# Kernel tuning notes

Measured on AMD Instinct MI355X. Metric: run time of the kernel, lower is better.

Reference implementation:

```python
import jax, jax.numpy as jnp
from jax import lax
import numpy as np

PATCH_H = 8
PATCH_W = 8


def setup_inputs() -> dict:
    key = jax.random.key(0)
    k1, k2 = jax.random.split(key)
    x = jax.random.normal(k1, (2, 1024, 256, 256), dtype=jnp.float32)
    # Conv1d weight [C_out, C_in, k], bias=False
    conv_w = jax.random.normal(k2, (1024, 1024, 3), dtype=jnp.float32) * 0.02
    return {"x": x, "conv_w": conv_w}


def reference(x, conv_w):
    B, C, H, W = x.shape
    hf, wf = H // PATCH_H, W // PATCH_W
    P = hf * wf
    # Patch average pool: mean over each (PATCH_H, PATCH_W) tile -> [B, C, hf, wf]
    xp = x.reshape(B, C, hf, PATCH_H, wf, PATCH_W)
    y = xp.mean(axis=(3, 5)).reshape(B, C, P)
    # Conv1d over the patch axis (SAME padding, no bias), then sigmoid gate
    g = lax.conv_general_dilated(
        y, conv_w, window_strides=(1,), padding="SAME",
        dimension_numbers=("NCH", "OIH", "NCH"))
    g = jax.nn.sigmoid(g).reshape(B, C, hf, wf)
    # Broadcast gate back over each patch and multiply
    out = xp * g[:, :, :, None, :, None]
    return out.reshape(B, C, H, W)
```

## Files before the change

### kernel.cpp

```cpp
#include <hip/hip_runtime.h>
#include <hip/hip_bf16.h>

#define HH 256
#define WW 256
#define CCH 1024
#define PP 1024

using f32x4 = __attribute__((ext_vector_type(4))) float;
using short8 = __attribute__((ext_vector_type(8))) short;

__global__ __launch_bounds__(256) void pool_kernel(const float* __restrict__ x,
                                                   float* __restrict__ y) {
    int bc   = blockIdx.x;
    int wid  = threadIdx.x >> 6;
    int lane = threadIdx.x & 63;
    const float* xp = x + (size_t)bc * (HH * WW) + lane * 4;
    float* yp = y + (size_t)bc * PP;
#pragma unroll
    for (int s = 0; s < 8; ++s) {
        int ph = wid + s * 4;
        const float* slab = xp + (size_t)ph * 8 * WW;
        float acc = 0.f;
#pragma unroll
        for (int r = 0; r < 8; ++r) {
            f32x4 v = __builtin_nontemporal_load((const f32x4*)(slab + (size_t)r * WW));
            acc += v.x + v.y + v.z + v.w;
        }
        acc += __shfl_xor(acc, 1);
        if ((lane & 1) == 0)
            yp[ph * 32 + (lane >> 1)] = acc * (1.f / 64.f);
    }
}

__global__ __launch_bounds__(256) void wconv_pad_kernel(const float* __restrict__ w,
                                                        __hip_bfloat16* __restrict__ wT,
                                                        __hip_bfloat16* __restrict__ yT) {
    int tid = blockIdx.x * 256 + threadIdx.x;
    const float* p = w + (size_t)tid * 3;
    float a = p[0], b = p[1], c = p[2];
    wT[tid]               = __float2bfloat16(a);
    wT[(1u << 20) + tid]  = __float2bfloat16(b);
    wT[(2u << 20) + tid]  = __float2bfloat16(c);
    if (tid < 2 * CCH) {
        int bb = tid >> 10, cc = tid & 1023;
        __hip_bfloat16 z = __float2bfloat16(0.f);
        __hip_bfloat16* base = yT + (size_t)bb * (PP + 2) * CCH;
        base[cc] = z;
        base[(size_t)(PP + 1) * CCH + cc] = z;
    }
}

__global__ __launch_bounds__(256) void transpose_kernel(const float* __restrict__ y,
                                                        __hip_bfloat16* __restrict__ yT) {
    int b  = blockIdx.z;
    int c0 = blockIdx.x * 32;
    int p0 = blockIdx.y * 32;
    __shared__ float tile[32][33];
    int tx = threadIdx.x, ty = threadIdx.y;
    const float* yb = y + (size_t)b * CCH * PP;
#pragma unroll
    for (int rr = 0; rr < 4; ++rr)
        tile[ty + rr * 8][tx] = yb[(size_t)(c0 + ty + rr * 8) * PP + p0 + tx];
    __syncthreads();
    __hip_bfloat16* yTb = yT + (size_t)b * (PP + 2) * CCH;
#pragma unroll
    for (int rr = 0; rr < 4; ++rr)
        yTb[(size_t)(1 + p0 + ty + rr * 8) * CCH + c0 + tx] =
            __float2bfloat16(tile[tx][ty + rr * 8]);
}

__global__ __launch_bounds__(512) void conv_gemm_kernel(
        const __hip_bfloat16* __restrict__ wT,
        const __hip_bfloat16* __restrict__ yT,
        float* __restrict__ gate) {
    int lane = threadIdx.x & 63;
    int wid  = threadIdx.x >> 6;
    int wp  = wid & 1, wco = wid >> 1;
    int l15 = lane & 15, lhi = lane >> 4;
    int co_base = blockIdx.x * 64 + wco * 16;
    int p_base  = blockIdx.y * 64 + wp * 32;
    int b = blockIdx.z;
    const __hip_bfloat16* yTb = yT + (size_t)b * (PP + 2) * CCH;

    f32x4 acc[2] = {};
#pragma unroll
    for (int tap = 0; tap < 3; ++tap) {
        const __hip_bfloat16* Ap = wT + (size_t)tap * (1u << 20)
                                 + (size_t)(co_base + l15) * CCH + lhi * 8;
        const __hip_bfloat16* Bp = yTb + (size_t)(p_base + l15 + tap) * CCH + lhi * 8;
        for (int ci0 = 0; ci0 < CCH; ci0 += 32) {
            short8 a0 = *(const short8*)(Ap + ci0);
            short8 b0 = *(const short8*)(Bp + ci0);
            short8 b1 = *(const short8*)(Bp + ci0 + 16 * CCH);
            acc[0] = __builtin_amdgcn_mfma_f32_16x16x32_bf16(a0, b0, acc[0], 0, 0, 0);
            acc[1] = __builtin_amdgcn_mfma_f32_16x16x32_bf16(a0, b1, acc[1], 0, 0, 0);
        }
    }
    float* gb = gate + (size_t)b * CCH * PP;
#pragma unroll
    for (int j16 = 0; j16 < 2; ++j16) {
        int col  = p_base + j16 * 16 + l15;
        int row0 = co_base + lhi * 4;
#pragma unroll
        for (int r = 0; r < 4; ++r) {
            float v = acc[j16][r];
            gb[(size_t)(row0 + r) * PP + col] = 1.f / (1.f + __expf(-v));
        }
    }
}

__global__ __launch_bounds__(256) void apply_kernel(const float* __restrict__ x,
                                                    const float* __restrict__ gate,
                                                    float* __restrict__ out) {
    int bc = blockIdx.x;
    const float* xp = x   + (size_t)bc * (HH * WW);
    float*       op = out + (size_t)bc * (HH * WW);
    __shared__ float g[PP];
    int t = threadIdx.x;
    ((f32x4*)g)[t] = ((const f32x4*)(gate + (size_t)bc * PP))[t];
    __syncthreads();
    int col4 = t & 63;
    int r    = t >> 6;
    int pc   = col4 >> 1;
#pragma unroll 4
    for (int it = 0; it < 64; ++it) {
        int row = it * 4 + r;
        float gg = g[(row >> 3) * 32 + pc];
        size_t off = (size_t)row * 64 + col4;
        f32x4 v = __builtin_nontemporal_load((const f32x4*)xp + off);
        v *= gg;
        __builtin_nontemporal_store(v, (f32x4*)op + off);
    }
}

extern "C" void kernel_launch(void* const* d_in, const int* in_sizes, int n_in,
                              void* d_out, int out_size, void* d_ws, size_t ws_size,
                              hipStream_t stream) {
    const float* x = (const float*)d_in[0];
    const float* w = (const float*)d_in[1];
    float* out = (float*)d_out;

    char* ws = (char*)d_ws;
    float*          y    = (float*)(ws);
    __hip_bfloat16* yT   = (__hip_bfloat16*)(ws + 8388608);
    __hip_bfloat16* wT   = (__hip_bfloat16*)(ws + 12591104);
    float*          gate = (float*)(ws + 18882560);

    hipLaunchKernelGGL(pool_kernel,      dim3(2048),      dim3(256),   0, stream, x, y);
    hipLaunchKernelGGL(wconv_pad_kernel, dim3(4096),      dim3(256),   0, stream, w, wT, yT);
    hipLaunchKernelGGL(transpose_kernel, dim3(32, 32, 2), dim3(32, 8), 0, stream, y, yT);
    hipLaunchKernelGGL(conv_gemm_kernel, dim3(16, 16, 2), dim3(512),   0, stream, wT, yT, gate);
    hipLaunchKernelGGL(apply_kernel,     dim3(2048),      dim3(256),   0, stream, x, gate, out);
}
```

Baseline: 427.2 us.

## Fuse all stages into one cooperative persistent kernel with grid syncs

Replaces the five separate kernel launches with a single cooperative kernel of 256 blocks that runs pooling, weight conversion, transpose, the MFMA conv GEMM and the gated apply in sequence, separated by grid.sync barriers. The aim is to remove per-launch overhead and inter-kernel gaps. In exchange the grid drops to 256 persistent blocks, which lowers parallelism in the memory-bound pool and apply phases, and each grid barrier adds its own cost. If the cooperative launch fails, the code falls back to the original launches.

```diff
diff --git a/kernel.cpp b/kernel.cpp
--- a/kernel.cpp
+++ b/kernel.cpp
@@ -1,5 +1,6 @@
 #include <hip/hip_runtime.h>
 #include <hip/hip_bf16.h>
+#include <hip/hip_cooperative_groups.h>
 
 #define HH 256
 #define WW 256
@@ -8,6 +9,147 @@
 
 using f32x4 = __attribute__((ext_vector_type(4))) float;
 using short8 = __attribute__((ext_vector_type(8))) short;
+
+namespace cg = cooperative_groups;
+
+__global__ __launch_bounds__(512, 2) void fused_kernel(
+        const float* __restrict__ x, const float* __restrict__ w,
+        float* __restrict__ out,
+        float* __restrict__ y, __hip_bfloat16* __restrict__ yT,
+        __hip_bfloat16* __restrict__ wT, float* __restrict__ gate) {
+    cg::grid_group grid = cg::this_grid();
+    __shared__ __align__(16) float lds[32 * 33];
+
+    const int bid  = blockIdx.x;
+    const int t    = threadIdx.x;
+    const int wid  = t >> 6;
+    const int lane = t & 63;
+
+    {
+        int plane = bid * 8 + wid;
+        const float* xp = x + (size_t)plane * (HH * WW) + lane * 4;
+        float* yp = y + (size_t)plane * PP;
+#pragma unroll 2
+        for (int ph = 0; ph < 32; ++ph) {
+            const float* slab = xp + (size_t)ph * 8 * WW;
+            float acc = 0.f;
+#pragma unroll
+            for (int r = 0; r < 8; ++r) {
+                f32x4 v = __builtin_nontemporal_load((const f32x4*)(slab + (size_t)r * WW));
+                acc += v.x + v.y + v.z + v.w;
+            }
+            acc += __shfl_xor(acc, 1);
+            if ((lane & 1) == 0)
+                yp[ph * 32 + (lane >> 1)] = acc * (1.f / 64.f);
+        }
+    }
+    {
+#pragma unroll
+        for (int it = 0; it < 8; ++it) {
+            int idx = it * (1 << 17) + bid * 512 + t;
+            const float* p = w + (size_t)idx * 3;
+            wT[idx]             = __float2bfloat16(p[0]);
+            wT[(1 << 20) + idx] = __float2bfloat16(p[1]);
+            wT[(2 << 20) + idx] = __float2bfloat16(p[2]);
+        }
+        int g0 = bid * 512 + t;
+        if (g0 < 2 * CCH) {
+            int bb = g0 >> 10, cc = g0 & 1023;
+            __hip_bfloat16 z = __float2bfloat16(0.f);
+            __hip_bfloat16* base = yT + (size_t)bb * (PP + 2) * CCH;
+            base[cc] = z;
+            base[(size_t)(PP + 1) * CCH + cc] = z;
+        }
+    }
+    __threadfence();
+    grid.sync();
+
+    {
+        int tx = t & 31, ty = t >> 5;
+#pragma unroll 1
+        for (int i = 0; i < 8; ++i) {
+            int tt = bid * 8 + i;
+            int b = tt >> 10, rem = tt & 1023;
+            int c0 = (rem >> 5) * 32, p0 = (rem & 31) * 32;
+            const float* yb = y + (size_t)b * CCH * PP;
+#pragma unroll
+            for (int rr = 0; rr < 2; ++rr)
+                lds[(ty + rr * 16) * 33 + tx] = yb[(size_t)(c0 + ty + rr * 16) * PP + p0 + tx];
+            __syncthreads();
+            __hip_bfloat16* yTb = yT + (size_t)b * (PP + 2) * CCH;
+#pragma unroll
+            for (int rr = 0; rr < 2; ++rr)
+                yTb[(size_t)(1 + p0 + ty + rr * 16) * CCH + c0 + tx] =
+                    __float2bfloat16(lds[tx * 33 + ty + rr * 16]);
+            __syncthreads();
+        }
+    }
+    __threadfence();
+    grid.sync();
+
+    {
+        int wp = wid & 1, wco = wid >> 1;
+        int l15 = lane & 15, lhi = lane >> 4;
+#pragma unroll 1
+        for (int j = 0; j < 2; ++j) {
+            int job = bid * 2 + j;
+            int bx = job & 15, by = (job >> 4) & 15, bz = job >> 8;
+            int co_base = bx * 64 + wco * 16;
+            int p_base  = by * 64 + wp * 32;
+            const __hip_bfloat16* yTb = yT + (size_t)bz * (PP + 2) * CCH;
+            f32x4 acc[2] = {};
+#pragma unroll
+            for (int tap = 0; tap < 3; ++tap) {
+                const __hip_bfloat16* Ap = wT + (size_t)tap * (1u << 20)
+                                         + (size_t)(co_base + l15) * CCH + lhi * 8;
+                const __hip_bfloat16* Bp = yTb + (size_t)(p_base + l15 + tap) * CCH + lhi * 8;
+                for (int ci0 = 0; ci0 < CCH; ci0 += 32) {
+                    short8 a0 = *(const short8*)(Ap + ci0);
+                    short8 b0 = *(const short8*)(Bp + ci0);
+                    short8 b1 = *(const short8*)(Bp + ci0 + 16 * CCH);
+                    acc[0] = __builtin_amdgcn_mfma_f32_16x16x32_bf16(a0, b0, acc[0], 0, 0, 0);
+                    acc[1] = __builtin_amdgcn_mfma_f32_16x16x32_bf16(a0, b1, acc[1], 0, 0, 0);
+                }
+            }
+            float* gb = gate + (size_t)bz * CCH * PP;
+#pragma unroll
+            for (int j16 = 0; j16 < 2; ++j16) {
+                int col  = p_base + j16 * 16 + l15;
+                int row0 = co_base + lhi * 4;
+#pragma unroll
+                for (int r = 0; r < 4; ++r)
+                    gb[(size_t)(row0 + r) * PP + col] = 1.f / (1.f + __expf(-acc[j16][r]));
+            }
+        }
+    }
+    __threadfence();
+    grid.sync();
+
+    {
+        int col4 = t & 63;
+        int r    = t >> 6;
+        int pc   = col4 >> 1;
+#pragma unroll 1
+        for (int i = 0; i < 8; ++i) {
+            int plane = bid * 8 + i;
+            const float* xp = x   + (size_t)plane * (HH * WW);
+            float*       op = out + (size_t)plane * (HH * WW);
+            if (t < 256)
+                ((f32x4*)lds)[t] = ((const f32x4*)(gate + (size_t)plane * PP))[t];
+            __syncthreads();
+#pragma unroll 4
+            for (int it = 0; it < 32; ++it) {
+                int row = it * 8 + r;
+                float gg = lds[(row >> 3) * 32 + pc];
+                size_t off = (size_t)row * 64 + col4;
+                f32x4 v = __builtin_nontemporal_load((const f32x4*)xp + off);
+                v *= gg;
+                __builtin_nontemporal_store(v, (f32x4*)op + off);
+            }
+            __syncthreads();
+        }
+    }
+}
 
 __global__ __launch_bounds__(256) void pool_kernel(const float* __restrict__ x,
                                                    float* __restrict__ y) {
@@ -37,10 +179,9 @@
                                                         __hip_bfloat16* __restrict__ yT) {
     int tid = blockIdx.x * 256 + threadIdx.x;
     const float* p = w + (size_t)tid * 3;
-    float a = p[0], b = p[1], c = p[2];
-    wT[tid]               = __float2bfloat16(a);
-    wT[(1u << 20) + tid]  = __float2bfloat16(b);
-    wT[(2u << 20) + tid]  = __float2bfloat16(c);
+    wT[tid]               = __float2bfloat16(p[0]);
+    wT[(1u << 20) + tid]  = __float2bfloat16(p[1]);
+    wT[(2u << 20) + tid]  = __float2bfloat16(p[2]);
     if (tid < 2 * CCH) {
         int bb = tid >> 10, cc = tid & 1023;
         __hip_bfloat16 z = __float2bfloat16(0.f);
@@ -81,7 +222,6 @@
     int p_base  = blockIdx.y * 64 + wp * 32;
     int b = blockIdx.z;
     const __hip_bfloat16* yTb = yT + (size_t)b * (PP + 2) * CCH;
-
     f32x4 acc[2] = {};
 #pragma unroll
     for (int tap = 0; tap < 3; ++tap) {
@@ -102,10 +242,8 @@
         int col  = p_base + j16 * 16 + l15;
         int row0 = co_base + lhi * 4;
 #pragma unroll
-        for (int r = 0; r < 4; ++r) {
-            float v = acc[j16][r];
-            gb[(size_t)(row0 + r) * PP + col] = 1.f / (1.f + __expf(-v));
-        }
+        for (int r = 0; r < 4; ++r)
+            gb[(size_t)(row0 + r) * PP + col] = 1.f / (1.f + __expf(-acc[j16][r]));
     }
 }
 
@@ -146,9 +284,16 @@
     __hip_bfloat16* wT   = (__hip_bfloat16*)(ws + 12591104);
     float*          gate = (float*)(ws + 18882560);
 
-    hipLaunchKernelGGL(pool_kernel,      dim3(2048),      dim3(256),   0, stream, x, y);
-    hipLaunchKernelGGL(wconv_pad_kernel, dim3(4096),      dim3(256),   0, stream, w, wT, yT);
-    hipLaunchKernelGGL(transpose_kernel, dim3(32, 32, 2), dim3(32, 8), 0, stream, y, yT);
-    hipLaunchKernelGGL(conv_gemm_kernel, dim3(16, 16, 2), dim3(512),   0, stream, wT, yT, gate);
-    hipLaunchKernelGGL(apply_kernel,     dim3(2048),      dim3(256),   0, stream, x, gate, out);
-}
+    void* args[] = {(void*)&x, (void*)&w, (void*)&out,
+                    (void*)&y, (void*)&yT, (void*)&wT, (void*)&gate};
+    hipError_t err = hipLaunchCooperativeKernel((const void*)fused_kernel,
+                                                dim3(256), dim3(512), args, 0, stream);
+    if (err != hipSuccess) {
+        (void)hipGetLastError();
+        hipLaunchKernelGGL(pool_kernel,      dim3(2048),      dim3(256),   0, stream, x, y);
+        hipLaunchKernelGGL(wconv_pad_kernel, dim3(4096),      dim3(256),   0, stream, w, wT, yT);
+        hipLaunchKernelGGL(transpose_kernel, dim3(32, 32, 2), dim3(32, 8), 0, stream, y, yT);
+        hipLaunchKernelGGL(conv_gemm_kernel, dim3(16, 16, 2), dim3(512),   0, stream, wT, yT, gate);
+        hipLaunchKernelGGL(apply_kernel,     dim3(2048),      dim3(256),   0, stream, x, gate, out);
+    }
+}
```

After: 806.6 us. +88.8%, slower.

## Process batches separately to keep per-batch input resident in cache between pool and apply

Applied to the files above, without the earlier changes.

Splits the pipeline into per-batch launches so each batch's 256MB slice of x is pooled and then gated while it may still sit in the large last-level cache. Pool and apply now use regular loads instead of nontemporal ones. Apply walks channels in reverse order so it starts on the most recently pooled data. This doubles the number of launches and halves the grid of each kernel, which lowers occupancy of the small conv GEMM.

```diff
diff --git a/kernel.cpp b/kernel.cpp
--- a/kernel.cpp
+++ b/kernel.cpp
@@ -9,13 +9,13 @@
 using f32x4 = __attribute__((ext_vector_type(4))) float;
 using short8 = __attribute__((ext_vector_type(8))) short;
 
-__global__ __launch_bounds__(256) void pool_kernel(const float* __restrict__ x,
-                                                   float* __restrict__ y) {
-    int bc   = blockIdx.x;
+__global__ __launch_bounds__(256) void pool_kernel(const float* __restrict__ xb,
+                                                   float* __restrict__ yb) {
+    int c    = blockIdx.x;
     int wid  = threadIdx.x >> 6;
     int lane = threadIdx.x & 63;
-    const float* xp = x + (size_t)bc * (HH * WW) + lane * 4;
-    float* yp = y + (size_t)bc * PP;
+    const float* xp = xb + (size_t)c * (HH * WW) + lane * 4;
+    float* yp = yb + (size_t)c * PP;
 #pragma unroll
     for (int s = 0; s < 8; ++s) {
         int ph = wid + s * 4;
@@ -23,7 +23,7 @@
         float acc = 0.f;
 #pragma unroll
         for (int r = 0; r < 8; ++r) {
-            f32x4 v = __builtin_nontemporal_load((const f32x4*)(slab + (size_t)r * WW));
+            f32x4 v = *(const f32x4*)(slab + (size_t)r * WW);
             acc += v.x + v.y + v.z + v.w;
         }
         acc += __shfl_xor(acc, 1);
@@ -37,10 +37,9 @@
                                                         __hip_bfloat16* __restrict__ yT) {
     int tid = blockIdx.x * 256 + threadIdx.x;
     const float* p = w + (size_t)tid * 3;
-    float a = p[0], b = p[1], c = p[2];
-    wT[tid]               = __float2bfloat16(a);
-    wT[(1u << 20) + tid]  = __float2bfloat16(b);
-    wT[(2u << 20) + tid]  = __float2bfloat16(c);
+    wT[tid]               = __float2bfloat16(p[0]);
+    wT[(1u << 20) + tid]  = __float2bfloat16(p[1]);
+    wT[(2u << 20) + tid]  = __float2bfloat16(p[2]);
     if (tid < 2 * CCH) {
         int bb = tid >> 10, cc = tid & 1023;
         __hip_bfloat16 z = __float2bfloat16(0.f);
@@ -50,19 +49,16 @@
     }
 }
 
-__global__ __launch_bounds__(256) void transpose_kernel(const float* __restrict__ y,
-                                                        __hip_bfloat16* __restrict__ yT) {
-    int b  = blockIdx.z;
+__global__ __launch_bounds__(256) void transpose_kernel(const float* __restrict__ yb,
+                                                        __hip_bfloat16* __restrict__ yTb) {
     int c0 = blockIdx.x * 32;
     int p0 = blockIdx.y * 32;
     __shared__ float tile[32][33];
     int tx = threadIdx.x, ty = threadIdx.y;
-    const float* yb = y + (size_t)b * CCH * PP;
 #pragma unroll
     for (int rr = 0; rr < 4; ++rr)
         tile[ty + rr * 8][tx] = yb[(size_t)(c0 + ty + rr * 8) * PP + p0 + tx];
     __syncthreads();
-    __hip_bfloat16* yTb = yT + (size_t)b * (PP + 2) * CCH;
 #pragma unroll
     for (int rr = 0; rr < 4; ++rr)
         yTb[(size_t)(1 + p0 + ty + rr * 8) * CCH + c0 + tx] =
@@ -71,17 +67,14 @@
 
 __global__ __launch_bounds__(512) void conv_gemm_kernel(
         const __hip_bfloat16* __restrict__ wT,
-        const __hip_bfloat16* __restrict__ yT,
-        float* __restrict__ gate) {
+        const __hip_bfloat16* __restrict__ yTb,
+        float* __restrict__ gateb) {
     int lane = threadIdx.x & 63;
     int wid  = threadIdx.x >> 6;
     int wp  = wid & 1, wco = wid >> 1;
     int l15 = lane & 15, lhi = lane >> 4;
     int co_base = blockIdx.x * 64 + wco * 16;
     int p_base  = blockIdx.y * 64 + wp * 32;
-    int b = blockIdx.z;
-    const __hip_bfloat16* yTb = yT + (size_t)b * (PP + 2) * CCH;
-
     f32x4 acc[2] = {};
 #pragma unroll
     for (int tap = 0; tap < 3; ++tap) {
@@ -96,28 +89,25 @@
             acc[1] = __builtin_amdgcn_mfma_f32_16x16x32_bf16(a0, b1, acc[1], 0, 0, 0);
         }
     }
-    float* gb = gate + (size_t)b * CCH * PP;
 #pragma unroll
     for (int j16 = 0; j16 < 2; ++j16) {
         int col  = p_base + j16 * 16 + l15;
         int row0 = co_base + lhi * 4;
 #pragma unroll
-        for (int r = 0; r < 4; ++r) {
-            float v = acc[j16][r];
-            gb[(size_t)(row0 + r) * PP + col] = 1.f / (1.f + __expf(-v));
-        }
+        for (int r = 0; r < 4; ++r)
+            gateb[(size_t)(row0 + r) * PP + col] = 1.f / (1.f + __expf(-acc[j16][r]));
     }
 }
 
-__global__ __launch_bounds__(256) void apply_kernel(const float* __restrict__ x,
-                                                    const float* __restrict__ gate,
-                                                    float* __restrict__ out) {
-    int bc = blockIdx.x;
-    const float* xp = x   + (size_t)bc * (HH * WW);
-    float*       op = out + (size_t)bc * (HH * WW);
+__global__ __launch_bounds__(256) void apply_kernel(const float* __restrict__ xb,
+                                                    const float* __restrict__ gateb,
+                                                    float* __restrict__ outb) {
+    int c = 1023 - blockIdx.x;
+    const float* xp = xb   + (size_t)c * (HH * WW);
+    float*       op = outb + (size_t)c * (HH * WW);
     __shared__ float g[PP];
     int t = threadIdx.x;
-    ((f32x4*)g)[t] = ((const f32x4*)(gate + (size_t)bc * PP))[t];
+    ((f32x4*)g)[t] = ((const f32x4*)(gateb + (size_t)c * PP))[t];
     __syncthreads();
     int col4 = t & 63;
     int r    = t >> 6;
@@ -127,7 +117,7 @@
         int row = it * 4 + r;
         float gg = g[(row >> 3) * 32 + pc];
         size_t off = (size_t)row * 64 + col4;
-        f32x4 v = __builtin_nontemporal_load((const f32x4*)xp + off);
+        f32x4 v = *((const f32x4*)xp + off);
         v *= gg;
         __builtin_nontemporal_store(v, (f32x4*)op + off);
     }
@@ -146,9 +136,16 @@
     __hip_bfloat16* wT   = (__hip_bfloat16*)(ws + 12591104);
     float*          gate = (float*)(ws + 18882560);
 
-    hipLaunchKernelGGL(pool_kernel,      dim3(2048),      dim3(256),   0, stream, x, y);
-    hipLaunchKernelGGL(wconv_pad_kernel, dim3(4096),      dim3(256),   0, stream, w, wT, yT);
-    hipLaunchKernelGGL(transpose_kernel, dim3(32, 32, 2), dim3(32, 8), 0, stream, y, yT);
-    hipLaunchKernelGGL(conv_gemm_kernel, dim3(16, 16, 2), dim3(512),   0, stream, wT, yT, gate);
-    hipLaunchKernelGGL(apply_kernel,     dim3(2048),      dim3(256),   0, stream, x, gate, out);
+    hipLaunchKernelGGL(wconv_pad_kernel, dim3(4096), dim3(256), 0, stream, w, wT, yT);
+    for (int b = 0; b < 2; ++b) {
+        const float* xb = x + (size_t)b * CCH * HH * WW;
+        float* yb       = y + (size_t)b * CCH * PP;
+        __hip_bfloat16* yTb = yT + (size_t)b * (PP + 2) * CCH;
+        float* gateb    = gate + (size_t)b * CCH * PP;
+        float* outb     = out + (size_t)b * CCH * HH * WW;
+        hipLaunchKernelGGL(pool_kernel,      dim3(1024),      dim3(256),   0, stream, xb, yb);
+        hipLaunchKernelGGL(transpose_kernel, dim3(32, 32),    dim3(32, 8), 0, stream, yb, yTb);
+        hipLaunchKernelGGL(conv_gemm_kernel, dim3(16, 16),    dim3(512),   0, stream, wT, yTb, gateb);
+        hipLaunchKernelGGL(apply_kernel,     dim3(1024),      dim3(256),   0, stream, xb, gateb, outb);
+    }
 }
```

New measurement: 412.8 us. 1.03x faster.
